# Kernel optimization log

Measured on AMD Instinct MI355X. Metric: run time of the kernel, lower is better.

The kernel has to match this reference:

```python
import jax, jax.numpy as jnp
import numpy as np

H, B, T, C = 1024, 256, 256, 10

def setup_inputs() -> dict:
    key = jax.random.key(0)
    ks = jax.random.split(key, 10)
    def xav(k, shape):
        fan_in, fan_out = shape[1], shape[0]
        lim = jnp.sqrt(6.0 / (fan_in + fan_out))
        return jax.random.uniform(k, shape, jnp.float32, -lim, lim)
    return {
        "x": jax.random.normal(ks[0], (B, T), jnp.float32),
        "W_gx": xav(ks[1], (H, 1)), "W_gh": xav(ks[2], (H, H)),
        "W_ix": xav(ks[3], (H, 1)), "W_ih": xav(ks[4], (H, H)),
        "W_fx": xav(ks[5], (H, 1)), "W_fh": xav(ks[6], (H, H)),
        "W_ox": xav(ks[7], (H, 1)), "W_oh": xav(ks[8], (H, H)),
        "W_ph": xav(ks[9], (C, H)),
        "b_g": jnp.zeros((B,), jnp.float32), "b_i": jnp.zeros((B,), jnp.float32),
        "b_f": jnp.zeros((B,), jnp.float32), "b_o": jnp.zeros((B,), jnp.float32),
        "b_p": jnp.zeros((B,), jnp.float32),
    }

def reference(x, W_gx, W_gh, W_ix, W_ih, W_fx, W_fh, W_ox, W_oh, W_ph,
              b_g, b_i, b_f, b_o, b_p):
    batch = x.shape[0]
    hidden = W_gh.shape[0]
    xs = x.T  # [T, B]; per-step x_t is a [1, B] row (input_dim = 1)

    def step(carry, x_t):
        h, c = carry                       # [H, B] each
        xr = x_t[None, :]                  # [1, B]
        g = jnp.tanh(W_gx @ xr + W_gh @ h + b_g)          # [H, B] + [B] broadcasts per column
        i = jax.nn.sigmoid(W_ix @ xr + W_ih @ h + b_i)
        f = jax.nn.sigmoid(W_fx @ xr + W_fh @ h + b_f)
        o = jax.nn.sigmoid(W_ox @ xr + W_oh @ h + b_o)
        c_new = g * i + c * f
        h_new = jnp.tanh(c_new) * o
        return (h_new, c_new), None

    h0 = jnp.zeros((hidden, batch), x.dtype)
    c0 = jnp.zeros((hidden, batch), x.dtype)
    (h_T, _), _ = jax.lax.scan(step, (h0, c0), xs)
    p = W_ph @ h_T + b_p                   # [C, B]
    y = jax.nn.softmax(p, axis=1)          # faithful: softmax over dim=1 (batch axis)
    return y.T                             # [B, C]
```

## Files before the change

### kernel.cpp

```cpp
#include <hip/hip_runtime.h>
#include <hip/hip_bf16.h>


#define H 1024
#define B 256
#define T 256
#define NCLS 10

typedef __attribute__((ext_vector_type(8))) short short8;
typedef __attribute__((ext_vector_type(2))) float f32x2;
typedef __attribute__((ext_vector_type(4))) float f32x4;
typedef __attribute__((ext_vector_type(16))) float f32x16;

__device__ inline unsigned short bf16_bits(float f) {
    union { __hip_bfloat16 h; unsigned short u; } cv;
    cv.h = __float2bfloat16(f);
    return cv.u;
}

#define L2E 1.4426950408889634f
__device__ inline float sigm_fast(float x) {
    float e = __builtin_amdgcn_exp2f(-L2E * x);
    return __builtin_amdgcn_rcpf(1.0f + e);
}
__device__ inline float tanh_fast(float x) {
    float e = __builtin_amdgcn_exp2f((2.0f * L2E) * x);
    return 1.0f - 2.0f * __builtin_amdgcn_rcpf(1.0f + e);
}


#define LOADS4(d0, d1, d2, d3, PTR, SC)                                   \
    __asm__ volatile(                                                     \
        "global_load_dwordx4 %0, %4, off " SC "\n\t"                      \
        "global_load_dwordx4 %1, %4, off offset:1024 " SC "\n\t"          \
        "global_load_dwordx4 %2, %4, off offset:2048 " SC "\n\t"          \
        "global_load_dwordx4 %3, %4, off offset:3072 " SC                  \
        : "=&v"(d0), "=&v"(d1), "=&v"(d2), "=&v"(d3)                      \
        : "v"(PTR));

#define WAIT4(N, d0, d1, d2, d3)                                          \
    __asm__ volatile("s_waitcnt vmcnt(" N ")"                             \
        : "+v"(d0), "+v"(d1), "+v"(d2), "+v"(d3));

#define MM(c, bb)                                                         \
    acc0 = __builtin_amdgcn_mfma_f32_32x32x16_bf16(awreg[0][c], bb, acc0, 0, 0, 0); \
    acc1 = __builtin_amdgcn_mfma_f32_32x32x16_bf16(awreg[1][c], bb, acc1, 0, 0, 0);

#define GATE_MFMA(SC)                                                     \
    {                                                                     \
        short8 b0, b1, b2, b3, b4, b5, b6, b7;                            \
        short8 b8, b9, b10, b11, b12, b13, b14, b15;                      \
        LOADS4(b0, b1, b2, b3, gb, SC)                                    \
        LOADS4(b4, b5, b6, b7, gb + 4096, SC)                             \
        WAIT4("4", b0, b1, b2, b3)                                        \
        MM(0, b0) MM(1, b1) MM(2, b2) MM(3, b3)                           \
        LOADS4(b8, b9, b10, b11, gb + 8192, SC)                           \
        LOADS4(b12, b13, b14, b15, gb + 12288, SC)                        \
        WAIT4("8", b4, b5, b6, b7)                                        \
        MM(4, b4) MM(5, b5) MM(6, b6) MM(7, b7)                           \
        WAIT4("4", b8, b9, b10, b11)                                      \
        MM(8, b8) MM(9, b9) MM(10, b10) MM(11, b11)                       \
        WAIT4("0", b12, b13, b14, b15)                                    \
        MM(12, b12) MM(13, b13) MM(14, b14) MM(15, b15)                   \
    }

__global__ __launch_bounds__(512)
__attribute__((amdgpu_waves_per_eu(2, 2)))
void lstm_persist(
    const float* __restrict__ x,
    const float* __restrict__ Wgh, const float* __restrict__ Wih,
    const float* __restrict__ Wfh, const float* __restrict__ Woh,
    const float* __restrict__ Wgx, const float* __restrict__ Wix,
    const float* __restrict__ Wfx, const float* __restrict__ Wox,
    const float* __restrict__ bg, const float* __restrict__ bi,
    const float* __restrict__ bf_, const float* __restrict__ bo,
    char* __restrict__ frag,
    unsigned* __restrict__ flags,
    unsigned* __restrict__ det,
    float* __restrict__ hfin)
{
    __shared__ __align__(16) float zb[16][32][32];
    __shared__ float wxl[4][32];
    __shared__ float bsl[4][32];
    __shared__ int sh_lcl;

    const int tid  = threadIdx.x;
    const int lane = tid & 63;
    const int wave = tid >> 6;
    const int gp   = wave >> 2;
    const int kq   = wave & 3;
    const int bt = blockIdx.x & 7;
    const int jt = blockIdx.x >> 3;
    const int j0 = jt * 32;
    const int b0 = bt * 32;

    unsigned xcc;
    __asm__ volatile("s_getreg_b32 %0, hwreg(HW_REG_XCC_ID)" : "=s"(xcc));
    xcc &= 7u;
    if (tid == 0)
        __hip_atomic_store(&det[bt * 32 + jt], xcc + 1u,
                           __ATOMIC_RELAXED, __HIP_MEMORY_SCOPE_AGENT);

    if (tid < 128) {
        int g = tid >> 5, r = tid & 31;
        const float* wx = (g == 0) ? Wgx : (g == 1) ? Wix : (g == 2) ? Wfx : Wox;
        const float* bb = (g == 0) ? bg  : (g == 1) ? bi  : (g == 2) ? bf_ : bo;
        wxl[g][r] = wx[j0 + r];
        bsl[g][r] = bb[b0 + r];
    }

    const float* Wlo = (gp == 0) ? Wgh : Wfh;
    const float* Whi = (gp == 0) ? Wih : Woh;
    short8 awreg[2][16];
#pragma unroll
    for (int gg = 0; gg < 2; ++gg) {
        const float* Wp = gg ? Whi : Wlo;
        const float* wrow = Wp + (j0 + (lane & 31)) * H
                          + kq * 256 + ((lane >> 5) * 8);
#pragma unroll
        for (int c = 0; c < 16; ++c) {
            const float4 f0 = *(const float4*)(wrow + c * 16);
            const float4 f1 = *(const float4*)(wrow + c * 16 + 4);
            short8 s;
            s[0] = (short)bf16_bits(f0.x); s[1] = (short)bf16_bits(f0.y);
            s[2] = (short)bf16_bits(f0.z); s[3] = (short)bf16_bits(f0.w);
            s[4] = (short)bf16_bits(f1.x); s[5] = (short)bf16_bits(f1.y);
            s[6] = (short)bf16_bits(f1.z); s[7] = (short)bf16_bits(f1.w);
            awreg[gg][c] = s;
        }
    }
#pragma unroll
    for (int gg = 0; gg < 2; ++gg)
#pragma unroll
        for (int c = 0; c < 16; ++c)
            __asm__ volatile("" : "+a"(awreg[gg][c]));

    if (wave == 0) {
        unsigned v;
        while (true) {
            v = __hip_atomic_load(&det[bt * 32 + (lane & 31)],
                                  __ATOMIC_RELAXED, __HIP_MEMORY_SCOPE_AGENT);
            if (__all((int)(v != 0u))) break;
            __builtin_amdgcn_s_sleep(1);
        }
        int same = __all((int)(v == xcc + 1u));
        if (tid == 0) sh_lcl = same;
    }
    __syncthreads();
    const bool lcl = (sh_lcl != 0);

    float creg[2] = {0.f, 0.f};
    const int nn = tid & 31;
    const int aa = tid >> 5;

    unsigned* myflag = &flags[blockIdx.x * 32];
    unsigned* pollflag = &flags[(((kq << 3) + (lane & 7)) * 8 + bt) * 32];

    for (int t = 0; t < T; ++t) {
        const float xv = x[(b0 + nn) * T + t];

        f32x16 acc0 = {0.f,0.f,0.f,0.f,0.f,0.f,0.f,0.f,
                       0.f,0.f,0.f,0.f,0.f,0.f,0.f,0.f};
        f32x16 acc1 = acc0;

        if (t > 0) {
            {
                const unsigned target = (unsigned)t;
                while (true) {
                    unsigned v = __hip_atomic_load(pollflag, __ATOMIC_RELAXED,
                                                   __HIP_MEMORY_SCOPE_AGENT);
                    if (__all((int)(v >= target))) break;
                    __builtin_amdgcn_s_sleep(1);
                }
            }
            __asm__ volatile("" :: "v"(xv));

            const char* gb = frag + (t & 1) * 524288 + bt * 65536
                           + (kq << 14) + lane * 16;
            if (lcl) {
                GATE_MFMA("sc0")
            } else {
                GATE_MFMA("sc0 sc1")
            }
        }

        {
            float* zbF = &zb[0][0][0];
            const int col = lane & 31;
            const int hi  = lane >> 5;
            const int g0 = gp * 2, g1 = g0 + 1;
#pragma unroll
            for (int rq = 0; rq < 4; ++rq) {
                const int sw = ((2 * rq + hi) ^ (col & 7)) << 2;
                f32x4 w0, w1;
#pragma unroll
                for (int e = 0; e < 4; ++e) {
                    w0[e] = acc0[rq * 4 + e];
                    w1[e] = acc1[rq * 4 + e];
                }
                *(f32x4*)(zbF + ((kq * 4 + g0) << 10) + (col << 5) + sw) = w0;
                *(f32x4*)(zbF + ((kq * 4 + g1) << 10) + (col << 5) + sw) = w1;
            }
        }
        __syncthreads();

        {
            const int grp = aa >> 1, half = aa & 1;
            const float* zcol = &zb[0][0][0] + (nn << 5);
            const int fo = ((grp ^ (nn & 7)) << 2) + (half << 1);
            f32x2 zs[4];
#pragma unroll
            for (int gi = 0; gi < 4; ++gi) {
                f32x2 s = *(const f32x2*)(zcol + (gi << 10) + fo);
#pragma unroll
                for (int kk = 1; kk < 4; ++kk)
                    s += *(const f32x2*)(zcol + (((kk << 2) + gi) << 10) + fo);
                zs[gi] = s;
            }
            unsigned short hb[2];
#pragma unroll
            for (int q = 0; q < 2; ++q) {
                const int jl = 2 * aa + q;
                float zg = zs[0][q] + wxl[0][jl] * xv + bsl[0][nn];
                float zi = zs[1][q] + wxl[1][jl] * xv + bsl[1][nn];
                float zf = zs[2][q] + wxl[2][jl] * xv + bsl[2][nn];
                float zo = zs[3][q] + wxl[3][jl] * xv + bsl[3][nn];
                float g  = tanh_fast(zg);
                float ig = sigm_fast(zi);
                float fg = sigm_fast(zf);
                float og = sigm_fast(zo);
                creg[q] = g * ig + creg[q] * fg;
                float hn = tanh_fast(creg[q]) * og;
                hb[q] = bf16_bits(hn);
                if (t == T - 1) hfin[(j0 + jl) * B + (b0 + nn)] = hn;
            }
            const unsigned val = (unsigned)hb[0] | ((unsigned)hb[1] << 16);
            const int jj = j0 + 2 * aa;
            short* fb = (short*)(frag + ((t + 1) & 1) * 524288) + bt * 32768;
            short* fdst = fb + (jj >> 4) * 512 + ((jj >> 3) & 1) * 256
                        + nn * 8 + (jj & 7);
            if (lcl) {
                __asm__ volatile("global_store_dword %0, %1, off"
                                 :: "v"(fdst), "v"(val) : "memory");
            } else {
                __hip_atomic_store((unsigned*)fdst, val, __ATOMIC_RELAXED,
                                   __HIP_MEMORY_SCOPE_AGENT);
            }
        }

        __syncthreads();
        if (tid == 0) {
            __asm__ volatile("s_waitcnt vmcnt(0)" ::: "memory");
            __hip_atomic_store(myflag, (unsigned)(t + 1), __ATOMIC_RELAXED,
                               __HIP_MEMORY_SCOPE_AGENT);
        }
    }
}

__global__ __launch_bounds__(256) void lstm_final(
    const float* __restrict__ Wph, const float* __restrict__ hfin,
    const float* __restrict__ bp, float* __restrict__ out)
{
    __shared__ float sh[256];
    __shared__ float shm, shs;
    int c = blockIdx.x;
    int b = threadIdx.x;
    float acc = bp[b];
    const float* wr = Wph + c * H;
    for (int k = 0; k < H; ++k)
        acc += wr[k] * hfin[k * B + b];

    sh[b] = acc;
    __syncthreads();
    for (int s = 128; s > 0; s >>= 1) {
        if (b < s) sh[b] = fmaxf(sh[b], sh[b + s]);
        __syncthreads();
    }
    if (b == 0) shm = sh[0];
    __syncthreads();
    float e = expf(acc - shm);
    sh[b] = e;
    __syncthreads();
    for (int s = 128; s > 0; s >>= 1) {
        if (b < s) sh[b] += sh[b + s];
        __syncthreads();
    }
    if (b == 0) shs = sh[0];
    __syncthreads();
    out[b * NCLS + c] = e / shs;
}

extern "C" void kernel_launch(void* const* d_in, const int* in_sizes, int n_in,
                              void* d_out, int out_size, void* d_ws, size_t ws_size,
                              hipStream_t stream)
{
    const float* x   = (const float*)d_in[0];
    const float* Wgx = (const float*)d_in[1];
    const float* Wgh = (const float*)d_in[2];
    const float* Wix = (const float*)d_in[3];
    const float* Wih = (const float*)d_in[4];
    const float* Wfx = (const float*)d_in[5];
    const float* Wfh = (const float*)d_in[6];
    const float* Wox = (const float*)d_in[7];
    const float* Woh = (const float*)d_in[8];
    const float* Wph = (const float*)d_in[9];
    const float* bg  = (const float*)d_in[10];
    const float* bi  = (const float*)d_in[11];
    const float* bfv = (const float*)d_in[12];
    const float* bo  = (const float*)d_in[13];
    const float* bp  = (const float*)d_in[14];

    char* ws = (char*)d_ws;
    char* frag = ws;
    unsigned* flags = (unsigned*)(ws + 1048576);
    unsigned* det   = (unsigned*)(ws + 1081344);
    float* hfin = (float*)(ws + 1085440);

    hipMemsetAsync(flags, 0, 36864, stream);

    lstm_persist<<<256, 512, 0, stream>>>(
        x, Wgh, Wih, Wfh, Woh, Wgx, Wix, Wfx, Wox,
        bg, bi, bfv, bo, frag, flags, det, hfin);

    lstm_final<<<NCLS, 256, 0, stream>>>(Wph, hfin, bp, (float*)d_out);
}
```

Before: 1.107 ms.

## Split K across eight waves with all four gates per wave

Each of the 8 waves now takes a 128-wide K slice and computes all four gate tiles, where before waves were split into two gate pairs across four 256-wide K quarters. Every wave now loads only half as many h fragments (8 instead of 16) per step and issues four independent MFMA chains, which shortens the load-to-MFMA critical path and gives more independent accumulators. The cost is a larger LDS reduction buffer (8 partials per gate instead of 4), more LDS writes and reads in the reduction, and four live accumulators per wave. Polling now reads flags from the 4 producer blocks matching the new 128-wide K slice instead of 8.

Measured after the change: 1.144 ms. 3.4% more time.

```diff
diff --git a/kernel.cpp b/kernel.cpp
--- a/kernel.cpp
+++ b/kernel.cpp
@@ -42,26 +42,21 @@
     __asm__ volatile("s_waitcnt vmcnt(" N ")"                             \
         : "+v"(d0), "+v"(d1), "+v"(d2), "+v"(d3));
 
-#define MM(c, bb)                                                         \
-    acc0 = __builtin_amdgcn_mfma_f32_32x32x16_bf16(awreg[0][c], bb, acc0, 0, 0, 0); \
-    acc1 = __builtin_amdgcn_mfma_f32_32x32x16_bf16(awreg[1][c], bb, acc1, 0, 0, 0);
-
-#define GATE_MFMA(SC)                                                     \
+#define MM4(c, bb)                                                        \
+    a0 = __builtin_amdgcn_mfma_f32_32x32x16_bf16(awreg[0][c], bb, a0, 0, 0, 0); \
+    a1 = __builtin_amdgcn_mfma_f32_32x32x16_bf16(awreg[1][c], bb, a1, 0, 0, 0); \
+    a2 = __builtin_amdgcn_mfma_f32_32x32x16_bf16(awreg[2][c], bb, a2, 0, 0, 0); \
+    a3 = __builtin_amdgcn_mfma_f32_32x32x16_bf16(awreg[3][c], bb, a3, 0, 0, 0);
+
+#define GATE_MFMA8(SC)                                                    \
     {                                                                     \
         short8 b0, b1, b2, b3, b4, b5, b6, b7;                            \
-        short8 b8, b9, b10, b11, b12, b13, b14, b15;                      \
         LOADS4(b0, b1, b2, b3, gb, SC)                                    \
         LOADS4(b4, b5, b6, b7, gb + 4096, SC)                             \
         WAIT4("4", b0, b1, b2, b3)                                        \
-        MM(0, b0) MM(1, b1) MM(2, b2) MM(3, b3)                           \
-        LOADS4(b8, b9, b10, b11, gb + 8192, SC)                           \
-        LOADS4(b12, b13, b14, b15, gb + 12288, SC)                        \
-        WAIT4("8", b4, b5, b6, b7)                                        \
-        MM(4, b4) MM(5, b5) MM(6, b6) MM(7, b7)                           \
-        WAIT4("4", b8, b9, b10, b11)                                      \
-        MM(8, b8) MM(9, b9) MM(10, b10) MM(11, b11)                       \
-        WAIT4("0", b12, b13, b14, b15)                                    \
-        MM(12, b12) MM(13, b13) MM(14, b14) MM(15, b15)                   \
+        MM4(0, b0) MM4(1, b1) MM4(2, b2) MM4(3, b3)                       \
+        WAIT4("0", b4, b5, b6, b7)                                        \
+        MM4(4, b4) MM4(5, b5) MM4(6, b6) MM4(7, b7)                       \
     }
 
 __global__ __launch_bounds__(512)
@@ -79,16 +74,14 @@
     unsigned* __restrict__ det,
     float* __restrict__ hfin)
 {
-    __shared__ __align__(16) float zb[16][32][32];
+    __shared__ __align__(16) float zb[32][32][32];
     __shared__ float wxl[4][32];
     __shared__ float bsl[4][32];
     __shared__ int sh_lcl;
 
     const int tid  = threadIdx.x;
     const int lane = tid & 63;
-    const int wave = tid >> 6;
-    const int gp   = wave >> 2;
-    const int kq   = wave & 3;
+    const int ke   = tid >> 6;
     const int bt = blockIdx.x & 7;
     const int jt = blockIdx.x >> 3;
     const int j0 = jt * 32;
@@ -109,16 +102,14 @@
         bsl[g][r] = bb[b0 + r];
     }
 
-    const float* Wlo = (gp == 0) ? Wgh : Wfh;
-    const float* Whi = (gp == 0) ? Wih : Woh;
-    short8 awreg[2][16];
-#pragma unroll
-    for (int gg = 0; gg < 2; ++gg) {
-        const float* Wp = gg ? Whi : Wlo;
-        const float* wrow = Wp + (j0 + (lane & 31)) * H
-                          + kq * 256 + ((lane >> 5) * 8);
-#pragma unroll
-        for (int c = 0; c < 16; ++c) {
+    const float* Wptr[4] = {Wgh, Wih, Wfh, Woh};
+    short8 awreg[4][8];
+#pragma unroll
+    for (int g = 0; g < 4; ++g) {
+        const float* wrow = Wptr[g] + (j0 + (lane & 31)) * H
+                          + ke * 128 + ((lane >> 5) * 8);
+#pragma unroll
+        for (int c = 0; c < 8; ++c) {
             const float4 f0 = *(const float4*)(wrow + c * 16);
             const float4 f1 = *(const float4*)(wrow + c * 16 + 4);
             short8 s;
@@ -126,16 +117,16 @@
             s[2] = (short)bf16_bits(f0.z); s[3] = (short)bf16_bits(f0.w);
             s[4] = (short)bf16_bits(f1.x); s[5] = (short)bf16_bits(f1.y);
             s[6] = (short)bf16_bits(f1.z); s[7] = (short)bf16_bits(f1.w);
-            awreg[gg][c] = s;
-        }
-    }
-#pragma unroll
-    for (int gg = 0; gg < 2; ++gg)
-#pragma unroll
-        for (int c = 0; c < 16; ++c)
-            __asm__ volatile("" : "+a"(awreg[gg][c]));
-
-    if (wave == 0) {
+            awreg[g][c] = s;
+        }
+    }
+#pragma unroll
+    for (int g = 0; g < 4; ++g)
+#pragma unroll
+        for (int c = 0; c < 8; ++c)
+            __asm__ volatile("" : "+a"(awreg[g][c]));
+
+    if (tid < 64) {
         unsigned v;
         while (true) {
             v = __hip_atomic_load(&det[bt * 32 + (lane & 31)],
@@ -154,14 +145,14 @@
     const int aa = tid >> 5;
 
     unsigned* myflag = &flags[blockIdx.x * 32];
-    unsigned* pollflag = &flags[(((kq << 3) + (lane & 7)) * 8 + bt) * 32];
+    unsigned* pollflag = &flags[(((ke << 2) + (lane & 3)) * 8 + bt) * 32];
 
     for (int t = 0; t < T; ++t) {
         const float xv = x[(b0 + nn) * T + t];
 
-        f32x16 acc0 = {0.f,0.f,0.f,0.f,0.f,0.f,0.f,0.f,
-                       0.f,0.f,0.f,0.f,0.f,0.f,0.f,0.f};
-        f32x16 acc1 = acc0;
+        f32x16 a0 = {0.f,0.f,0.f,0.f,0.f,0.f,0.f,0.f,
+                     0.f,0.f,0.f,0.f,0.f,0.f,0.f,0.f};
+        f32x16 a1 = a0, a2 = a0, a3 = a0;
 
         if (t > 0) {
             {
@@ -176,11 +167,11 @@
             __asm__ volatile("" :: "v"(xv));
 
             const char* gb = frag + (t & 1) * 524288 + bt * 65536
-                           + (kq << 14) + lane * 16;
+                           + (ke << 13) + lane * 16;
             if (lcl) {
-                GATE_MFMA("sc0")
+                GATE_MFMA8("sc0")
             } else {
-                GATE_MFMA("sc0 sc1")
+                GATE_MFMA8("sc0 sc1")
             }
         }
 
@@ -188,18 +179,22 @@
             float* zbF = &zb[0][0][0];
             const int col = lane & 31;
             const int hi  = lane >> 5;
-            const int g0 = gp * 2, g1 = g0 + 1;
 #pragma unroll
             for (int rq = 0; rq < 4; ++rq) {
                 const int sw = ((2 * rq + hi) ^ (col & 7)) << 2;
-                f32x4 w0, w1;
+                f32x4 w0, w1, w2, w3;
 #pragma unroll
                 for (int e = 0; e < 4; ++e) {
-                    w0[e] = acc0[rq * 4 + e];
-                    w1[e] = acc1[rq * 4 + e];
+                    w0[e] = a0[rq * 4 + e];
+                    w1[e] = a1[rq * 4 + e];
+                    w2[e] = a2[rq * 4 + e];
+                    w3[e] = a3[rq * 4 + e];
                 }
-                *(f32x4*)(zbF + ((kq * 4 + g0) << 10) + (col << 5) + sw) = w0;
-                *(f32x4*)(zbF + ((kq * 4 + g1) << 10) + (col << 5) + sw) = w1;
+                const int pb = (ke << 2);
+                *(f32x4*)(zbF + ((pb + 0) << 10) + (col << 5) + sw) = w0;
+                *(f32x4*)(zbF + ((pb + 1) << 10) + (col << 5) + sw) = w1;
+                *(f32x4*)(zbF + ((pb + 2) << 10) + (col << 5) + sw) = w2;
+                *(f32x4*)(zbF + ((pb + 3) << 10) + (col << 5) + sw) = w3;
             }
         }
         __syncthreads();
@@ -213,7 +208,7 @@
             for (int gi = 0; gi < 4; ++gi) {
                 f32x2 s = *(const f32x2*)(zcol + (gi << 10) + fo);
 #pragma unroll
-                for (int kk = 1; kk < 4; ++kk)
+                for (int kk = 1; kk < 8; ++kk)
                     s += *(const f32x2*)(zcol + (((kk << 2) + gi) << 10) + fo);
                 zs[gi] = s;
             }
```

## Stage x in LDS and pipeline flag polling with two in-flight loads

Applied to the files above, without the earlier changes.

Preloads each block's 32x256 slice of x into shared memory once, so the per-step global load of x is replaced by an LDS read. The spin-wait on the producer flags now keeps two staggered uncached loads in flight per iteration, checking the first and then the second, to cut the latency of detecting that the previous step's h fragments are ready. This adds 32 KB of LDS per block, which may affect occupancy, and uses inline asm with manual vmcnt waits in the poll loop.

New measurement: 1.142 ms. 1.03x slower.

```diff
diff --git a/kernel.cpp b/kernel.cpp
--- a/kernel.cpp
+++ b/kernel.cpp
@@ -80,6 +80,7 @@
     float* __restrict__ hfin)
 {
     __shared__ __align__(16) float zb[16][32][32];
+    __shared__ __align__(16) float xl[T][32];
     __shared__ float wxl[4][32];
     __shared__ float bsl[4][32];
     __shared__ int sh_lcl;
@@ -109,6 +110,20 @@
         bsl[g][r] = bb[b0 + r];
     }
 
+    {
+        const int row = tid & 31;
+        const int t0  = (tid >> 5) * 16;
+        const float* xrow = x + (b0 + row) * T + t0;
+#pragma unroll
+        for (int i = 0; i < 16; i += 4) {
+            const float4 f = *(const float4*)(xrow + i);
+            xl[t0 + i + 0][row] = f.x;
+            xl[t0 + i + 1][row] = f.y;
+            xl[t0 + i + 2][row] = f.z;
+            xl[t0 + i + 3][row] = f.w;
+        }
+    }
+
     const float* Wlo = (gp == 0) ? Wgh : Wfh;
     const float* Whi = (gp == 0) ? Wih : Woh;
     short8 awreg[2][16];
@@ -157,7 +172,7 @@
     unsigned* pollflag = &flags[(((kq << 3) + (lane & 7)) * 8 + bt) * 32];
 
     for (int t = 0; t < T; ++t) {
-        const float xv = x[(b0 + nn) * T + t];
+        const float xv = xl[t][nn];
 
         f32x16 acc0 = {0.f,0.f,0.f,0.f,0.f,0.f,0.f,0.f,
                        0.f,0.f,0.f,0.f,0.f,0.f,0.f,0.f};
@@ -167,13 +182,22 @@
             {
                 const unsigned target = (unsigned)t;
                 while (true) {
-                    unsigned v = __hip_atomic_load(pollflag, __ATOMIC_RELAXED,
-                                                   __HIP_MEMORY_SCOPE_AGENT);
-                    if (__all((int)(v >= target))) break;
+                    unsigned a, b;
+                    __asm__ volatile(
+                        "global_load_dword %0, %2, off sc0 sc1\n\t"
+                        "s_sleep 2\n\t"
+                        "global_load_dword %1, %2, off sc0 sc1\n\t"
+                        "s_waitcnt vmcnt(1)"
+                        : "=&v"(a), "=&v"(b) : "v"(pollflag) : "memory");
+                    if (__all((int)(a >= target))) {
+                        __asm__ volatile("s_waitcnt vmcnt(0)" ::: "memory");
+                        break;
+                    }
+                    __asm__ volatile("s_waitcnt vmcnt(0)" : "+v"(b) :: "memory");
+                    if (__all((int)(b >= target))) break;
                     __builtin_amdgcn_s_sleep(1);
                 }
             }
-            __asm__ volatile("" :: "v"(xv));
 
             const char* gb = frag + (t & 1) * 524288 + bt * 65536
                            + (kq << 14) + lane * 16;
```
